# Kernel optimization log

Measured on AMD Instinct MI355X. Metric: run time of the kernel, lower is better.

The kernel has to match this reference:

```python
import jax, jax.numpy as jnp
import numpy as np

N = 100            # node_num
B = 8              # batch
H = 256            # node_feature_hidden_dim
FD, FL = 16, 16    # node_feature_dim, node_feature_len
OUT = 4            # edge_output_dim
E = N * (N - 1)    # 9900 directed edges (off-diagonal)
_off = np.ones((N, N)) - np.eye(N)
REC, SEND = np.where(_off)   # rel_rec one-hot rows = REC, rel_send = SEND
REC = jnp.asarray(REC, jnp.int32)
SEND = jnp.asarray(SEND, jnp.int32)
BN_EPS = 1e-5


def _mlp(x, w1, b1, w2, b2, g, beta):
    # Linear-ReLU-Linear-ReLU-BatchNorm1d (training-mode batch stats, dropout=0)
    h = jax.nn.relu(x @ w1 + b1)
    h = jax.nn.relu(h @ w2 + b2)
    b_, e_, f_ = h.shape
    hf = h.reshape(b_ * e_, f_)
    mu = hf.mean(0)
    var = hf.var(0)  # biased variance, as torch BN uses for normalization
    hn = (hf - mu) * jax.lax.rsqrt(var + BN_EPS) * g + beta
    return hn.reshape(b_, e_, f_)


def _node2edge(x):
    # gather form of rel_send @ x / rel_rec @ x, cat([senders, receivers])
    return jnp.concatenate([x[:, SEND, :], x[:, REC, :]], axis=2)


def _edge2node(x):
    # scatter form of rel_rec.T @ x; original divides by incoming.size(1) == N
    incoming = jnp.zeros((x.shape[0], N, x.shape[2]), x.dtype).at[:, REC, :].add(x)
    return incoming / N


def setup_inputs() -> dict:
    key = jax.random.key(0)
    ks = jax.random.split(key, 40)

    def rn(k, shape, s=0.05):
        return (jax.random.normal(k, shape) * s).astype(jnp.float32)

    inp = {
        'x': rn(ks[0], (B, N, FD, FL), 1.0),
        'h': rn(ks[1], (B, N, 8, 8), 1.0),
        't_nodes': N,
        't_edges': E,
        'nodes_mask': jnp.ones((N,), jnp.int32),
        'edges_mask': jnp.ones((E,), jnp.int32),
    }
    n_in = {'mlp1': FD * FL, 'mlp2': 2 * H, 'mlp3': H, 'mlp4': 3 * H}
    i = 2
    for name, nin in n_in.items():
        inp[name + '_w1'] = rn(ks[i], (nin, H)); i += 1
        inp[name + '_b1'] = jnp.full((H,), 0.1, jnp.float32)
        inp[name + '_w2'] = rn(ks[i], (H, H)); i += 1
        inp[name + '_b2'] = jnp.full((H,), 0.1, jnp.float32)
        inp[name + '_g'] = jnp.ones((H,), jnp.float32)
        inp[name + '_beta'] = jnp.zeros((H,), jnp.float32)
    inp['fc_w'] = rn(ks[i], (H, OUT)); i += 1
    inp['fc_b'] = jnp.full((OUT,), 0.1, jnp.float32)
    return inp


def reference(x, h, t_nodes, t_edges, nodes_mask, edges_mask,
              mlp1_w1, mlp1_b1, mlp1_w2, mlp1_b2, mlp1_g, mlp1_beta,
              mlp2_w1, mlp2_b1, mlp2_w2, mlp2_b2, mlp2_g, mlp2_beta,
              mlp3_w1, mlp3_b1, mlp3_w2, mlp3_b2, mlp3_g, mlp3_beta,
              mlp4_w1, mlp4_b1, mlp4_w2, mlp4_b2, mlp4_g, mlp4_beta,
              fc_w, fc_b):
    # h, t_nodes, t_edges, nodes_mask, edges_mask are unused by the original forward
    xx = x.reshape(x.shape[0], x.shape[1], -1).astype(jnp.float32)  # [B,N,FD*FL]
    xx = _mlp(xx, mlp1_w1, mlp1_b1, mlp1_w2, mlp1_b2, mlp1_g, mlp1_beta)  # [B,N,H]
    xe = _node2edge(xx)                                                   # [B,E,2H]
    xe = _mlp(xe, mlp2_w1, mlp2_b1, mlp2_w2, mlp2_b2, mlp2_g, mlp2_beta)  # [B,E,H]
    x_skip = xe
    xn = _edge2node(xe)                                                   # [B,N,H]
    xn = _mlp(xn, mlp3_w1, mlp3_b1, mlp3_w2, mlp3_b2, mlp3_g, mlp3_beta)
    xe2 = _node2edge(xn)                                                  # [B,E,2H]
    xc = jnp.concatenate([xe2, x_skip], axis=2)                           # [B,E,3H]
    xc = _mlp(xc, mlp4_w1, mlp4_b1, mlp4_w2, mlp4_b2, mlp4_g, mlp4_beta)  # [B,E,H]
    z_g = xc @ fc_w + fc_b                                                # [B,E,OUT]
    return z_g
```

## Files before the change

kernel.cpp:

```cpp
#include <hip/hip_runtime.h>
#include <hip/hip_bf16.h>

#define Nn 100
#define Bb 8
#define Hh 256
#define Ee 9900
#define RE 79200
#define RN 800
#define BN_EPS 1e-5f

typedef __attribute__((ext_vector_type(8))) unsigned short ushort8_t;
typedef __attribute__((ext_vector_type(4))) unsigned short ushort4_t;
typedef __attribute__((ext_vector_type(8))) short bf16x8;
typedef __attribute__((ext_vector_type(4))) float f32x4;

__device__ __forceinline__ float bf2f(unsigned short u){
  return __uint_as_float(((unsigned)u) << 16);
}
__device__ __forceinline__ unsigned short f2bf(float f){
  unsigned u = __float_as_uint(f);
  return (unsigned short)((u + 0x7fffu + ((u >> 16) & 1u)) >> 16);
}

__device__ __forceinline__ void affine_prologue(const float* __restrict__ stats,
    float cnt, const float* __restrict__ g, const float* __restrict__ beta,
    float* a, float* c, int tid){
  if (tid < 256){
    float inv = 1.0f / cnt;
    float mu  = stats[tid] * inv;
    float var = fmaxf(stats[256 + tid] * inv - mu * mu, 0.f);
    float aa  = g[tid] * rsqrtf(var + BN_EPS);
    a[tid] = aa;
    c[tid] = beta[tid] - mu * aa;
  }
}

__device__ __forceinline__ void gemm_f32(const float* IN, const float* __restrict__ W,
                                         float acc[8][4], int tr, int tc){
  for (int k = 0; k < 256; k += 4){
    float4 w0 = *(const float4*)(W + (size_t)(k+0)*256 + 4*tc);
    float4 w1 = *(const float4*)(W + (size_t)(k+1)*256 + 4*tc);
    float4 w2 = *(const float4*)(W + (size_t)(k+2)*256 + 4*tc);
    float4 w3 = *(const float4*)(W + (size_t)(k+3)*256 + 4*tc);
    #pragma unroll
    for (int rr = 0; rr < 8; rr++){
      float4 iv = *(const float4*)(IN + (tr*8+rr)*256 + k);
      acc[rr][0] += iv.x*w0.x + iv.y*w1.x + iv.z*w2.x + iv.w*w3.x;
      acc[rr][1] += iv.x*w0.y + iv.y*w1.y + iv.z*w2.y + iv.w*w3.y;
      acc[rr][2] += iv.x*w0.z + iv.y*w1.z + iv.z*w2.z + iv.w*w3.z;
      acc[rr][3] += iv.x*w0.w + iv.y*w1.w + iv.z*w2.w + iv.w*w3.w;
    }
  }
}

template<int KW>
__device__ __forceinline__ void mfma_gemm(const unsigned short* Alds,
    const unsigned short* __restrict__ Bf, f32x4 acc[2][4], int w, int lane){
  const int l15 = lane & 15, kg = lane >> 4;
  for (int ks = 0; ks < KW/32; ks++){
    int byte0 = ((l15*KW      + ks*32 + kg*8) * 2) ^ ((l15 & 7) << 4);
    int byte1 = (((16+l15)*KW + ks*32 + kg*8) * 2) ^ ((l15 & 7) << 4);
    bf16x8 a0 = *(const bf16x8*)((const char*)Alds + byte0);
    bf16x8 a1 = *(const bf16x8*)((const char*)Alds + byte1);
    const unsigned short* bp = Bf + ((size_t)(ks*16 + w*4)*64 + lane)*8;
    #pragma unroll
    for (int cf = 0; cf < 4; cf++){
      bf16x8 b = *(const bf16x8*)(bp + cf*64*8);
      acc[0][cf] = __builtin_amdgcn_mfma_f32_16x16x32_bf16(a0, b, acc[0][cf], 0,0,0);
      acc[1][cf] = __builtin_amdgcn_mfma_f32_16x16x32_bf16(a1, b, acc[1][cf], 0,0,0);
    }
  }
}

__device__ __forceinline__ void zero_acc(f32x4 acc[2][4]){
  #pragma unroll
  for (int i = 0; i < 2; i++)
    #pragma unroll
    for (int j = 0; j < 4; j++){
      f32x4 z = {0.f, 0.f, 0.f, 0.f};
      acc[i][j] = z;
    }
}

#define STATS_PUSH(statsp)                                   \
  __syncthreads();                                           \
  atomicAdd(&(statsp)[tid], red[tid]);                       \
  atomicAdd(&(statsp)[tid + 256], red[tid + 256]);

__global__ void k_wprep(const float* __restrict__ W, unsigned short* __restrict__ out,
                        int ktiles){
  int id = blockIdx.x * 256 + threadIdx.x;
  int total = ktiles * 16 * 64;
  if (id >= total) return;
  int lane = id & 63, tile = id >> 6;
  int tc = tile & 15, tk = tile >> 4;
  int kbase = tk*32 + (lane>>4)*8, col = tc*16 + (lane&15);
  ushort8_t o;
  #pragma unroll
  for (int j = 0; j < 8; j++) o[j] = f2bf(W[(size_t)(kbase+j)*256 + col]);
  *(ushort8_t*)(out + (size_t)id*8) = o;
}

__global__ __launch_bounds__(256,2) void k_mlp1(
    const float* __restrict__ x,
    const float* __restrict__ W1, const float* __restrict__ b1,
    const float* __restrict__ W2, const float* __restrict__ b2,
    float* __restrict__ h1, float* __restrict__ stats){
  __shared__ float IN[32*256];
  __shared__ float O1[32*256];
  __shared__ float red[512];
  int tid = threadIdx.x, tr = tid >> 6, tc = tid & 63;
  int r0 = blockIdx.x * 32;
  #pragma unroll
  for (int j = 0; j < 8; j++){
    int idx = tid*4 + j*1024;
    *(float4*)(IN + idx) = *(const float4*)(x + (size_t)r0*256 + idx);
  }
  red[tid] = 0.f; red[tid + 256] = 0.f;
  __syncthreads();
  float acc[8][4];
  #pragma unroll
  for (int rr = 0; rr < 8; rr++){ acc[rr][0]=acc[rr][1]=acc[rr][2]=acc[rr][3]=0.f; }
  gemm_f32(IN, W1, acc, tr, tc);
  {
    float4 bb = *(const float4*)(b1 + 4*tc);
    #pragma unroll
    for (int rr = 0; rr < 8; rr++){
      float4 o;
      o.x = fmaxf(acc[rr][0]+bb.x, 0.f);
      o.y = fmaxf(acc[rr][1]+bb.y, 0.f);
      o.z = fmaxf(acc[rr][2]+bb.z, 0.f);
      o.w = fmaxf(acc[rr][3]+bb.w, 0.f);
      *(float4*)(O1 + (tr*8+rr)*256 + 4*tc) = o;
    }
  }
  __syncthreads();
  #pragma unroll
  for (int rr = 0; rr < 8; rr++){ acc[rr][0]=acc[rr][1]=acc[rr][2]=acc[rr][3]=0.f; }
  gemm_f32(O1, W2, acc, tr, tc);
  {
    float4 bb = *(const float4*)(b2 + 4*tc);
    float ls0=0,ls1=0,ls2=0,ls3=0,lq0=0,lq1=0,lq2=0,lq3=0;
    #pragma unroll
    for (int rr = 0; rr < 8; rr++){
      float4 v;
      v.x = fmaxf(acc[rr][0]+bb.x, 0.f);
      v.y = fmaxf(acc[rr][1]+bb.y, 0.f);
      v.z = fmaxf(acc[rr][2]+bb.z, 0.f);
      v.w = fmaxf(acc[rr][3]+bb.w, 0.f);
      *(float4*)(h1 + ((size_t)(r0 + tr*8 + rr))*256 + 4*tc) = v;
      ls0+=v.x; lq0+=v.x*v.x; ls1+=v.y; lq1+=v.y*v.y;
      ls2+=v.z; lq2+=v.z*v.z; ls3+=v.w; lq3+=v.w*v.w;
    }
    atomicAdd(&red[4*tc+0], ls0); atomicAdd(&red[4*tc+1], ls1);
    atomicAdd(&red[4*tc+2], ls2); atomicAdd(&red[4*tc+3], ls3);
    atomicAdd(&red[256+4*tc+0], lq0); atomicAdd(&red[256+4*tc+1], lq1);
    atomicAdd(&red[256+4*tc+2], lq2); atomicAdd(&red[256+4*tc+3], lq3);
  }
  STATS_PUSH(stats)
}

__global__ __launch_bounds__(256,2) void k_mlp2(
    const float* __restrict__ h1, const float* __restrict__ stats1,
    const float* __restrict__ g1, const float* __restrict__ be1,
    const unsigned short* __restrict__ W1f, const float* __restrict__ b1,
    const unsigned short* __restrict__ W2f, const float* __restrict__ b2,
    unsigned short* __restrict__ h2, float* __restrict__ stats2){
  __shared__ unsigned short A[32*512];
  __shared__ unsigned short O1[32*256];
  __shared__ float ap[256], cp[256];
  __shared__ float red[512];
  int tid = threadIdx.x, w = tid >> 6, lane = tid & 63;
  int l15 = lane & 15, kg = lane >> 4;
  int r0 = blockIdx.x * 32;
  affine_prologue(stats1, (float)RN, g1, be1, ap, cp, tid);
  red[tid] = 0.f; red[tid + 256] = 0.f;
  __syncthreads();
  {
    int cb = (lane & 31) * 8, half = lane >> 5;
    float4 a0 = *(const float4*)(ap+cb), a1 = *(const float4*)(ap+cb+4);
    float4 c0 = *(const float4*)(cp+cb), c1 = *(const float4*)(cp+cb+4);
    #pragma unroll
    for (int rr = 0; rr < 8; rr++){
      int rl = w*8+rr, rg = r0 + rl;
      int b = rg / Ee, e = rg - b*Ee;
      int i = e / 99, kk = e - i*99;
      int snd = kk + (kk >= i);
      int node = half ? i : snd;
      const float* sp = h1 + ((size_t)(b*Nn + node))*256 + cb;
      float4 v0 = *(const float4*)sp, v1 = *(const float4*)(sp+4);
      ushort8_t o;
      o[0]=f2bf(v0.x*a0.x+c0.x); o[1]=f2bf(v0.y*a0.y+c0.y);
      o[2]=f2bf(v0.z*a0.z+c0.z); o[3]=f2bf(v0.w*a0.w+c0.w);
      o[4]=f2bf(v1.x*a1.x+c1.x); o[5]=f2bf(v1.y*a1.y+c1.y);
      o[6]=f2bf(v1.z*a1.z+c1.z); o[7]=f2bf(v1.w*a1.w+c1.w);
      int byte = ((rl*512 + half*256 + cb)*2) ^ ((rl&7)<<4);
      *(ushort8_t*)((char*)A + byte) = o;
    }
  }
  __syncthreads();
  f32x4 acc[2][4];
  zero_acc(acc);
  mfma_gemm<512>(A, W1f, acc, w, lane);
  {
    #pragma unroll
    for (int cf = 0; cf < 4; cf++){
      int col = w*64 + cf*16 + l15;
      float bb = b1[col];
      #pragma unroll
      for (int rf = 0; rf < 2; rf++){
        #pragma unroll
        for (int r = 0; r < 4; r++){
          int row = rf*16 + kg*4 + r;
          float v = fmaxf(acc[rf][cf][r] + bb, 0.f);
          int byte = ((row*256 + col)*2) ^ ((row&7)<<4);
          *(unsigned short*)((char*)O1 + byte) = f2bf(v);
        }
      }
    }
  }
  __syncthreads();
  f32x4 acc2[2][4];
  zero_acc(acc2);
  mfma_gemm<256>(O1, W2f, acc2, w, lane);
  {
    #pragma unroll
    for (int cf = 0; cf < 4; cf++){
      int col = w*64 + cf*16 + l15;
      float bb = b2[col];
      float ls = 0.f, lq = 0.f;
      #pragma unroll
      for (int rf = 0; rf < 2; rf++){
        #pragma unroll
        for (int r = 0; r < 4; r++){
          int row = rf*16 + kg*4 + r;
          float v = fmaxf(acc2[rf][cf][r] + bb, 0.f);
          h2[(size_t)(r0 + row)*256 + col] = f2bf(v);
          ls += v; lq += v*v;
        }
      }
      atomicAdd(&red[col], ls);
      atomicAdd(&red[256+col], lq);
    }
  }
  STATS_PUSH(stats2)
}

__global__ __launch_bounds__(256,2) void k_mlp3(
    const unsigned short* __restrict__ h2, const float* __restrict__ stats2,
    const float* __restrict__ g2, const float* __restrict__ be2,
    const float* __restrict__ W1, const float* __restrict__ b1,
    const float* __restrict__ W2, const float* __restrict__ b2,
    float* __restrict__ h3, float* __restrict__ stats3){
  __shared__ float IN[32*256];
  __shared__ float O1[32*256];
  __shared__ float red[512];
  __shared__ float ap[256], cp[256];
  int tid = threadIdx.x, tr = tid >> 6, lane = tid & 63, tc = lane;
  int r0 = blockIdx.x * 32;
  affine_prologue(stats2, (float)RE, g2, be2, ap, cp, tid);
  red[tid] = 0.f; red[tid + 256] = 0.f;
  __syncthreads();
  {
    int cb = lane * 4;
    float4 av = *(const float4*)(ap+cb), cv = *(const float4*)(cp+cb);
    #pragma unroll
    for (int rr = 0; rr < 8; rr++){
      int m = r0 + tr*8 + rr;
      int b = m / Nn, i = m - b*Nn;
      const unsigned short* base = h2 + ((size_t)(b*Ee + i*99))*256 + cb;
      float s0=0,s1=0,s2=0,s3=0;
      for (int j = 0; j < 99; j++){
        ushort4_t hv = *(const ushort4_t*)(base + (size_t)j*256);
        s0 += bf2f(hv[0]); s1 += bf2f(hv[1]);
        s2 += bf2f(hv[2]); s3 += bf2f(hv[3]);
      }
      float4 o;
      o.x = (s0*av.x + 99.f*cv.x) * 0.01f;
      o.y = (s1*av.y + 99.f*cv.y) * 0.01f;
      o.z = (s2*av.z + 99.f*cv.z) * 0.01f;
      o.w = (s3*av.w + 99.f*cv.w) * 0.01f;
      *(float4*)(IN + (tr*8+rr)*256 + cb) = o;
    }
  }
  __syncthreads();
  float acc[8][4];
  #pragma unroll
  for (int rr = 0; rr < 8; rr++){ acc[rr][0]=acc[rr][1]=acc[rr][2]=acc[rr][3]=0.f; }
  gemm_f32(IN, W1, acc, tr, tc);
  {
    float4 bb = *(const float4*)(b1 + 4*tc);
    #pragma unroll
    for (int rr = 0; rr < 8; rr++){
      float4 o;
      o.x = fmaxf(acc[rr][0]+bb.x, 0.f);
      o.y = fmaxf(acc[rr][1]+bb.y, 0.f);
      o.z = fmaxf(acc[rr][2]+bb.z, 0.f);
      o.w = fmaxf(acc[rr][3]+bb.w, 0.f);
      *(float4*)(O1 + (tr*8+rr)*256 + 4*tc) = o;
    }
  }
  __syncthreads();
  #pragma unroll
  for (int rr = 0; rr < 8; rr++){ acc[rr][0]=acc[rr][1]=acc[rr][2]=acc[rr][3]=0.f; }
  gemm_f32(O1, W2, acc, tr, tc);
  {
    float4 bb = *(const float4*)(b2 + 4*tc);
    float ls0=0,ls1=0,ls2=0,ls3=0,lq0=0,lq1=0,lq2=0,lq3=0;
    #pragma unroll
    for (int rr = 0; rr < 8; rr++){
      float4 v;
      v.x = fmaxf(acc[rr][0]+bb.x, 0.f);
      v.y = fmaxf(acc[rr][1]+bb.y, 0.f);
      v.z = fmaxf(acc[rr][2]+bb.z, 0.f);
      v.w = fmaxf(acc[rr][3]+bb.w, 0.f);
      *(float4*)(h3 + ((size_t)(r0 + tr*8 + rr))*256 + 4*tc) = v;
      ls0+=v.x; lq0+=v.x*v.x; ls1+=v.y; lq1+=v.y*v.y;
      ls2+=v.z; lq2+=v.z*v.z; ls3+=v.w; lq3+=v.w*v.w;
    }
    atomicAdd(&red[4*tc+0], ls0); atomicAdd(&red[4*tc+1], ls1);
    atomicAdd(&red[4*tc+2], ls2); atomicAdd(&red[4*tc+3], ls3);
    atomicAdd(&red[256+4*tc+0], lq0); atomicAdd(&red[256+4*tc+1], lq1);
    atomicAdd(&red[256+4*tc+2], lq2); atomicAdd(&red[256+4*tc+3], lq3);
  }
  STATS_PUSH(stats3)
}

__global__ __launch_bounds__(256,2) void k_mlp4(
    const float* __restrict__ h3, const unsigned short* __restrict__ h2,
    const float* __restrict__ stats3, const float* __restrict__ g3, const float* __restrict__ be3,
    const float* __restrict__ stats2, const float* __restrict__ g2, const float* __restrict__ be2,
    const unsigned short* __restrict__ W1f, const float* __restrict__ b1,
    const unsigned short* __restrict__ W2f, const float* __restrict__ b2,
    unsigned short* __restrict__ h4, float* __restrict__ stats4){
  __shared__ unsigned short A[32*768];
  __shared__ unsigned short O1[32*256];
  __shared__ float a3[256], c3[256], a2[256], c2[256];
  __shared__ float red[512];
  int tid = threadIdx.x, w = tid >> 6, lane = tid & 63;
  int l15 = lane & 15, kg = lane >> 4;
  int r0 = blockIdx.x * 32;
  affine_prologue(stats3, (float)RN, g3, be3, a3, c3, tid);
  affine_prologue(stats2, (float)RE, g2, be2, a2, c2, tid);
  red[tid] = 0.f; red[tid + 256] = 0.f;
  __syncthreads();
  {
    int cb = (lane & 31) * 8, half = lane >> 5;
    float4 a0 = *(const float4*)(a3+cb), a1 = *(const float4*)(a3+cb+4);
    float4 c0 = *(const float4*)(c3+cb), c1 = *(const float4*)(c3+cb+4);
    #pragma unroll
    for (int rr = 0; rr < 8; rr++){
      int rl = w*8+rr, rg = r0 + rl;
      int b = rg / Ee, e = rg - b*Ee;
      int i = e / 99, kk = e - i*99;
      int snd = kk + (kk >= i);
      int node = half ? i : snd;
      const float* sp = h3 + ((size_t)(b*Nn + node))*256 + cb;
      float4 v0 = *(const float4*)sp, v1 = *(const float4*)(sp+4);
      ushort8_t o;
      o[0]=f2bf(v0.x*a0.x+c0.x); o[1]=f2bf(v0.y*a0.y+c0.y);
      o[2]=f2bf(v0.z*a0.z+c0.z); o[3]=f2bf(v0.w*a0.w+c0.w);
      o[4]=f2bf(v1.x*a1.x+c1.x); o[5]=f2bf(v1.y*a1.y+c1.y);
      o[6]=f2bf(v1.z*a1.z+c1.z); o[7]=f2bf(v1.w*a1.w+c1.w);
      int byte = ((rl*768 + half*256 + cb)*2) ^ ((rl&7)<<4);
      *(ushort8_t*)((char*)A + byte) = o;
    }
  }
  {
    int cb = lane * 4;
    float4 av = *(const float4*)(a2+cb), cv = *(const float4*)(c2+cb);
    #pragma unroll
    for (int rr = 0; rr < 8; rr++){
      int rl = w*8+rr, rg = r0 + rl;
      ushort4_t hv = *(const ushort4_t*)(h2 + (size_t)rg*256 + cb);
      ushort4_t o;
      o[0]=f2bf(bf2f(hv[0])*av.x+cv.x);
      o[1]=f2bf(bf2f(hv[1])*av.y+cv.y);
      o[2]=f2bf(bf2f(hv[2])*av.z+cv.z);
      o[3]=f2bf(bf2f(hv[3])*av.w+cv.w);
      int byte = ((rl*768 + 512 + cb)*2) ^ ((rl&7)<<4);
      *(ushort4_t*)((char*)A + byte) = o;
    }
  }
  __syncthreads();
  f32x4 acc[2][4];
  zero_acc(acc);
  mfma_gemm<768>(A, W1f, acc, w, lane);
  {
    #pragma unroll
    for (int cf = 0; cf < 4; cf++){
      int col = w*64 + cf*16 + l15;
      float bb = b1[col];
      #pragma unroll
      for (int rf = 0; rf < 2; rf++){
        #pragma unroll
        for (int r = 0; r < 4; r++){
          int row = rf*16 + kg*4 + r;
          float v = fmaxf(acc[rf][cf][r] + bb, 0.f);
          int byte = ((row*256 + col)*2) ^ ((row&7)<<4);
          *(unsigned short*)((char*)O1 + byte) = f2bf(v);
        }
      }
    }
  }
  __syncthreads();
  f32x4 acc2[2][4];
  zero_acc(acc2);
  mfma_gemm<256>(O1, W2f, acc2, w, lane);
  {
    #pragma unroll
    for (int cf = 0; cf < 4; cf++){
      int col = w*64 + cf*16 + l15;
      float bb = b2[col];
      float ls = 0.f, lq = 0.f;
      #pragma unroll
      for (int rf = 0; rf < 2; rf++){
        #pragma unroll
        for (int r = 0; r < 4; r++){
          int row = rf*16 + kg*4 + r;
          float v = fmaxf(acc2[rf][cf][r] + bb, 0.f);
          h4[(size_t)(r0 + row)*256 + col] = f2bf(v);
          ls += v; lq += v*v;
        }
      }
      atomicAdd(&red[col], ls);
      atomicAdd(&red[256+col], lq);
    }
  }
  STATS_PUSH(stats4)
}

__global__ __launch_bounds__(256,2) void k_out(
    const unsigned short* __restrict__ h4, const float* __restrict__ stats4,
    const float* __restrict__ g4, const float* __restrict__ be4,
    const float* __restrict__ fcw, const float* __restrict__ fcb,
    float* __restrict__ out){
  __shared__ unsigned short T[64*264];
  __shared__ float a4[256], c4[256], Wl[1024];
  int tid = threadIdx.x;
  affine_prologue(stats4, (float)RE, g4, be4, a4, c4, tid);
  #pragma unroll
  for (int j = 0; j < 4; j++){ int id = tid + j*256; Wl[id] = fcw[id]; }
  int r0 = blockIdx.x * 64;
  #pragma unroll
  for (int j = 0; j < 8; j++){
    int flat = tid + j*256;
    int rl = flat >> 5, cs = (flat & 31) * 8;
    ushort8_t v = {0,0,0,0,0,0,0,0};
    if (r0 + rl < RE) v = *(const ushort8_t*)(h4 + (size_t)(r0+rl)*256 + cs);
    *(ushort8_t*)(&T[rl*264 + cs]) = v;
  }
  __syncthreads();
  int row = tid >> 2, o = tid & 3;
  if (r0 + row < RE){
    float acc = fcb[o];
    for (int k = 0; k < 256; k += 8){
      ushort8_t iv = *(const ushort8_t*)(&T[row*264 + k]);
      #pragma unroll
      for (int kk = 0; kk < 8; kk++){
        float v = bf2f(iv[kk]) * a4[k+kk] + c4[k+kk];
        acc += v * Wl[(k+kk)*4 + o];
      }
    }
    out[(size_t)(r0+row)*4 + o] = acc;
  }
}

extern "C" void kernel_launch(void* const* d_in, const int* in_sizes, int n_in,
                              void* d_out, int out_size, void* d_ws, size_t ws_size,
                              hipStream_t stream){
  const float* x    = (const float*)d_in[0];
  const float* m1w1 = (const float*)d_in[6];  const float* m1b1 = (const float*)d_in[7];
  const float* m1w2 = (const float*)d_in[8];  const float* m1b2 = (const float*)d_in[9];
  const float* m1g  = (const float*)d_in[10]; const float* m1be = (const float*)d_in[11];
  const float* m2w1 = (const float*)d_in[12]; const float* m2b1 = (const float*)d_in[13];
  const float* m2w2 = (const float*)d_in[14]; const float* m2b2 = (const float*)d_in[15];
  const float* m2g  = (const float*)d_in[16]; const float* m2be = (const float*)d_in[17];
  const float* m3w1 = (const float*)d_in[18]; const float* m3b1 = (const float*)d_in[19];
  const float* m3w2 = (const float*)d_in[20]; const float* m3b2 = (const float*)d_in[21];
  const float* m3g  = (const float*)d_in[22]; const float* m3be = (const float*)d_in[23];
  const float* m4w1 = (const float*)d_in[24]; const float* m4b1 = (const float*)d_in[25];
  const float* m4w2 = (const float*)d_in[26]; const float* m4b2 = (const float*)d_in[27];
  const float* m4g  = (const float*)d_in[28]; const float* m4be = (const float*)d_in[29];
  const float* fcw  = (const float*)d_in[30]; const float* fcb  = (const float*)d_in[31];

  size_t need_bytes = (204800ull + 204800ull + 2048ull) * 4ull
                    + 2ull * (size_t)RE * 256ull * 2ull
                    + 458752ull * 2ull;
  if (ws_size < need_bytes) return;

  float* ws = (float*)d_ws;
  float* h1 = ws;
  float* h3 = ws + 204800;
  float* stats = ws + 409600;
  unsigned short* h2 = (unsigned short*)(stats + 2048);
  unsigned short* h4 = h2 + (size_t)RE * 256;
  unsigned short* w2a = h4 + (size_t)RE * 256;
  unsigned short* w2b = w2a + 512*256;
  unsigned short* w4a = w2b + 256*256;
  unsigned short* w4b = w4a + 768*256;

  hipMemsetAsync(stats, 0, 2048 * sizeof(float), stream);

  k_wprep<<<(16*16*64)/256, 256, 0, stream>>>(m2w1, w2a, 16);
  k_wprep<<<( 8*16*64)/256, 256, 0, stream>>>(m2w2, w2b, 8);
  k_wprep<<<(24*16*64)/256, 256, 0, stream>>>(m4w1, w4a, 24);
  k_wprep<<<( 8*16*64)/256, 256, 0, stream>>>(m4w2, w4b, 8);

  k_mlp1<<<RN/32, 256, 0, stream>>>(x, m1w1, m1b1, m1w2, m1b2, h1, stats);
  k_mlp2<<<RE/32, 256, 0, stream>>>(h1, stats, m1g, m1be,
                                    w2a, m2b1, w2b, m2b2, h2, stats + 512);
  k_mlp3<<<RN/32, 256, 0, stream>>>(h2, stats + 512, m2g, m2be,
                                    m3w1, m3b1, m3w2, m3b2, h3, stats + 1024);
  k_mlp4<<<RE/32, 256, 0, stream>>>(h3, h2, stats + 1024, m3g, m3be,
                                    stats + 512, m2g, m2be,
                                    w4a, m4b1, w4b, m4b2, h4, stats + 1536);
  k_out<<<(RE+63)/64, 256, 0, stream>>>(h4, stats + 1536, m4g, m4be,
                                        fcw, fcb, (float*)d_out);
}
```

Baseline: 498.2 us.

## Cut LDS use in edge MLPs for occupancy, split edge2node into its own kernel

The BN affine coefficients in k_mlp2 and k_mlp4 are now computed in registers from global stats instead of shared arrays. The O1 staging buffer reuses the A buffer after an added barrier. Together these shrink LDS so launch bounds can rise to 4 and 3 blocks per CU. The edge-to-node reduction, previously done serially inside the 25-block k_mlp3, moves to a separate 800-block kernel writing a float scratch buffer, which spreads that reduction across many more CUs. The cost is an extra launch and extra workspace, plus possible register-pressure spills under the tighter launch bounds.

```diff
diff --git a/kernel.cpp b/kernel.cpp
--- a/kernel.cpp
+++ b/kernel.cpp
@@ -35,6 +35,21 @@
   }
 }
 
+__device__ __forceinline__ void affine_reg(const float* __restrict__ stats,
+    float cnt, const float* __restrict__ g, const float* __restrict__ be,
+    int cb, float4& av, float4& cv){
+  float4 s = *(const float4*)(stats + cb);
+  float4 q = *(const float4*)(stats + 256 + cb);
+  float4 gg = *(const float4*)(g + cb);
+  float4 bb = *(const float4*)(be + cb);
+  float inv = 1.0f / cnt;
+  float mx = s.x*inv, my = s.y*inv, mz = s.z*inv, mw = s.w*inv;
+  av.x = gg.x * rsqrtf(fmaxf(q.x*inv - mx*mx, 0.f) + BN_EPS); cv.x = bb.x - mx*av.x;
+  av.y = gg.y * rsqrtf(fmaxf(q.y*inv - my*my, 0.f) + BN_EPS); cv.y = bb.y - my*av.y;
+  av.z = gg.z * rsqrtf(fmaxf(q.z*inv - mz*mz, 0.f) + BN_EPS); cv.z = bb.z - mz*av.z;
+  av.w = gg.w * rsqrtf(fmaxf(q.w*inv - mw*mw, 0.f) + BN_EPS); cv.w = bb.w - mw*av.w;
+}
+
 __device__ __forceinline__ void gemm_f32(const float* IN, const float* __restrict__ W,
                                          float acc[8][4], int tr, int tc){
   for (int k = 0; k < 256; k += 4){
@@ -160,26 +175,23 @@
   STATS_PUSH(stats)
 }
 
-__global__ __launch_bounds__(256,2) void k_mlp2(
+__global__ __launch_bounds__(256,4) void k_mlp2(
     const float* __restrict__ h1, const float* __restrict__ stats1,
     const float* __restrict__ g1, const float* __restrict__ be1,
     const unsigned short* __restrict__ W1f, const float* __restrict__ b1,
     const unsigned short* __restrict__ W2f, const float* __restrict__ b2,
     unsigned short* __restrict__ h2, float* __restrict__ stats2){
   __shared__ unsigned short A[32*512];
-  __shared__ unsigned short O1[32*256];
-  __shared__ float ap[256], cp[256];
   __shared__ float red[512];
   int tid = threadIdx.x, w = tid >> 6, lane = tid & 63;
   int l15 = lane & 15, kg = lane >> 4;
   int r0 = blockIdx.x * 32;
-  affine_prologue(stats1, (float)RN, g1, be1, ap, cp, tid);
   red[tid] = 0.f; red[tid + 256] = 0.f;
-  __syncthreads();
   {
     int cb = (lane & 31) * 8, half = lane >> 5;
-    float4 a0 = *(const float4*)(ap+cb), a1 = *(const float4*)(ap+cb+4);
-    float4 c0 = *(const float4*)(cp+cb), c1 = *(const float4*)(cp+cb+4);
+    float4 a0, c0, a1, c1;
+    affine_reg(stats1, (float)RN, g1, be1, cb,     a0, c0);
+    affine_reg(stats1, (float)RN, g1, be1, cb + 4, a1, c1);
     #pragma unroll
     for (int rr = 0; rr < 8; rr++){
       int rl = w*8+rr, rg = r0 + rl;
@@ -202,6 +214,8 @@
   f32x4 acc[2][4];
   zero_acc(acc);
   mfma_gemm<512>(A, W1f, acc, w, lane);
+  __syncthreads();
+  unsigned short* O1 = A;
   {
     #pragma unroll
     for (int cf = 0; cf < 4; cf++){
@@ -246,8 +260,20 @@
   STATS_PUSH(stats2)
 }
 
+__global__ __launch_bounds__(256,4) void k_e2n(
+    const unsigned short* __restrict__ h2, float* __restrict__ h3in){
+  int m = blockIdx.x;
+  int b = m / Nn, i = m - b*Nn;
+  int c = threadIdx.x;
+  const unsigned short* base = h2 + ((size_t)(b*Ee + i*99))*256 + c;
+  float s = 0.f;
+  #pragma unroll 4
+  for (int j = 0; j < 99; j++) s += bf2f(base[(size_t)j*256]);
+  h3in[(size_t)m*256 + c] = s;
+}
+
 __global__ __launch_bounds__(256,2) void k_mlp3(
-    const unsigned short* __restrict__ h2, const float* __restrict__ stats2,
+    const float* __restrict__ h3in, const float* __restrict__ stats2,
     const float* __restrict__ g2, const float* __restrict__ be2,
     const float* __restrict__ W1, const float* __restrict__ b1,
     const float* __restrict__ W2, const float* __restrict__ b2,
@@ -267,19 +293,12 @@
     #pragma unroll
     for (int rr = 0; rr < 8; rr++){
       int m = r0 + tr*8 + rr;
-      int b = m / Nn, i = m - b*Nn;
-      const unsigned short* base = h2 + ((size_t)(b*Ee + i*99))*256 + cb;
-      float s0=0,s1=0,s2=0,s3=0;
-      for (int j = 0; j < 99; j++){
-        ushort4_t hv = *(const ushort4_t*)(base + (size_t)j*256);
-        s0 += bf2f(hv[0]); s1 += bf2f(hv[1]);
-        s2 += bf2f(hv[2]); s3 += bf2f(hv[3]);
-      }
+      float4 s = *(const float4*)(h3in + (size_t)m*256 + cb);
       float4 o;
-      o.x = (s0*av.x + 99.f*cv.x) * 0.01f;
-      o.y = (s1*av.y + 99.f*cv.y) * 0.01f;
-      o.z = (s2*av.z + 99.f*cv.z) * 0.01f;
-      o.w = (s3*av.w + 99.f*cv.w) * 0.01f;
+      o.x = (s.x*av.x + 99.f*cv.x) * 0.01f;
+      o.y = (s.y*av.y + 99.f*cv.y) * 0.01f;
+      o.z = (s.z*av.z + 99.f*cv.z) * 0.01f;
+      o.w = (s.w*av.w + 99.f*cv.w) * 0.01f;
       *(float4*)(IN + (tr*8+rr)*256 + cb) = o;
     }
   }
@@ -326,7 +345,7 @@
   STATS_PUSH(stats3)
 }
 
-__global__ __launch_bounds__(256,2) void k_mlp4(
+__global__ __launch_bounds__(256,3) void k_mlp4(
     const float* __restrict__ h3, const unsigned short* __restrict__ h2,
     const float* __restrict__ stats3, const float* __restrict__ g3, const float* __restrict__ be3,
     const float* __restrict__ stats2, const float* __restrict__ g2, const float* __restrict__ be2,
@@ -334,20 +353,16 @@
     const unsigned short* __restrict__ W2f, const float* __restrict__ b2,
     unsigned short* __restrict__ h4, float* __restrict__ stats4){
   __shared__ unsigned short A[32*768];
-  __shared__ unsigned short O1[32*256];
-  __shared__ float a3[256], c3[256], a2[256], c2[256];
   __shared__ float red[512];
   int tid = threadIdx.x, w = tid >> 6, lane = tid & 63;
   int l15 = lane & 15, kg = lane >> 4;
   int r0 = blockIdx.x * 32;
-  affine_prologue(stats3, (float)RN, g3, be3, a3, c3, tid);
-  affine_prologue(stats2, (float)RE, g2, be2, a2, c2, tid);
   red[tid] = 0.f; red[tid + 256] = 0.f;
-  __syncthreads();
   {
     int cb = (lane & 31) * 8, half = lane >> 5;
-    float4 a0 = *(const float4*)(a3+cb), a1 = *(const float4*)(a3+cb+4);
-    float4 c0 = *(const float4*)(c3+cb), c1 = *(const float4*)(c3+cb+4);
+    float4 a0, c0, a1, c1;
+    affine_reg(stats3, (float)RN, g3, be3, cb,     a0, c0);
+    affine_reg(stats3, (float)RN, g3, be3, cb + 4, a1, c1);
     #pragma unroll
     for (int rr = 0; rr < 8; rr++){
       int rl = w*8+rr, rg = r0 + rl;
@@ -368,7 +383,8 @@
   }
   {
     int cb = lane * 4;
-    float4 av = *(const float4*)(a2+cb), cv = *(const float4*)(c2+cb);
+    float4 av, cv;
+    affine_reg(stats2, (float)RE, g2, be2, cb, av, cv);
     #pragma unroll
     for (int rr = 0; rr < 8; rr++){
       int rl = w*8+rr, rg = r0 + rl;
@@ -386,6 +402,8 @@
   f32x4 acc[2][4];
   zero_acc(acc);
   mfma_gemm<768>(A, W1f, acc, w, lane);
+  __syncthreads();
+  unsigned short* O1 = A;
   {
     #pragma unroll
     for (int cf = 0; cf < 4; cf++){
@@ -484,16 +502,17 @@
   const float* m4g  = (const float*)d_in[28]; const float* m4be = (const float*)d_in[29];
   const float* fcw  = (const float*)d_in[30]; const float* fcb  = (const float*)d_in[31];
 
-  size_t need_bytes = (204800ull + 204800ull + 2048ull) * 4ull
+  size_t need_bytes = (204800ull*3 + 2048ull) * 4ull
                     + 2ull * (size_t)RE * 256ull * 2ull
                     + 458752ull * 2ull;
   if (ws_size < need_bytes) return;
 
   float* ws = (float*)d_ws;
-  float* h1 = ws;
-  float* h3 = ws + 204800;
-  float* stats = ws + 409600;
-  unsigned short* h2 = (unsigned short*)(stats + 2048);
+  float* h1   = ws;
+  float* h3   = ws + 204800;
+  float* stats= ws + 409600;
+  float* h3in = ws + 411648;
+  unsigned short* h2 = (unsigned short*)(ws + 616448);
   unsigned short* h4 = h2 + (size_t)RE * 256;
   unsigned short* w2a = h4 + (size_t)RE * 256;
   unsigned short* w2b = w2a + 512*256;
@@ -510,7 +529,8 @@
   k_mlp1<<<RN/32, 256, 0, stream>>>(x, m1w1, m1b1, m1w2, m1b2, h1, stats);
   k_mlp2<<<RE/32, 256, 0, stream>>>(h1, stats, m1g, m1be,
                                     w2a, m2b1, w2b, m2b2, h2, stats + 512);
-  k_mlp3<<<RN/32, 256, 0, stream>>>(h2, stats + 512, m2g, m2be,
+  k_e2n<<<RN, 256, 0, stream>>>(h2, h3in);
+  k_mlp3<<<RN/32, 256, 0, stream>>>(h3in, stats + 512, m2g, m2be,
                                     m3w1, m3b1, m3w2, m3b2, h3, stats + 1024);
   k_mlp4<<<RE/32, 256, 0, stream>>>(h3, h2, stats + 1024, m3g, m3be,
                                     stats + 512, m2g, m2be,
```

After: 478.6 us. -3.9%, faster.
